# Kernel optimization log

Hardware: AMD Instinct MI355X
Metric: run time of the kernel (lower is better)

Reference implementation:

```python
import jax, jax.numpy as jnp
import numpy as np

B, T, C, H = 2, 2048, 1024, 16
HD = C // H  # head dim = 64


def setup_inputs() -> dict:
    key = jax.random.key(0)
    k1, k2, k3 = jax.random.split(key, 3)
    x = jax.random.normal(k1, (B, T, C), dtype=jnp.float32)
    W_attn = jax.random.normal(k2, (C, 3 * C), dtype=jnp.float32) * (C ** -0.5)
    W_proj = jax.random.normal(k3, (C, C), dtype=jnp.float32) * (C ** -0.5)
    b_proj = jnp.zeros((C,), dtype=jnp.float32)
    return {"x": x, "W_attn": W_attn, "W_proj": W_proj, "b_proj": b_proj}


def reference(x, W_attn, W_proj, b_proj):
    Bv, Tv, Cv = x.shape
    qkv = x @ W_attn  # [B, T, 3C]  (no bias: config.bias=False)
    # NOTE: source splits as k, q, v (k first!)
    k, q, v = jnp.split(qkv, 3, axis=2)
    # [B, H, T, HD]
    q = q.reshape(Bv, Tv, H, HD).transpose(0, 2, 1, 3)
    k = k.reshape(Bv, Tv, H, HD).transpose(0, 2, 1, 3)
    v = v.reshape(Bv, Tv, H, HD).transpose(0, 2, 1, 3)
    wei = jnp.einsum('bhqd,bhkd->bhqk', q, k) * (HD ** -0.5)
    causal = jnp.tril(jnp.ones((Tv, Tv), dtype=bool))
    wei = jnp.where(causal, wei, -jnp.inf)
    wei = jax.nn.softmax(wei, axis=-1)
    # dropout = 0.0 (eval) -> identity
    out = jnp.einsum('bhqk,bhkd->bhqd', wei, v)
    out = out.transpose(0, 2, 1, 3).reshape(Bv, Tv, Cv)
    out = out @ W_proj + b_proj
    return out
```

## Files before the change

### kernel.cpp

```cpp
#include <hip/hip_runtime.h>

typedef __attribute__((ext_vector_type(8))) short short8;
typedef __attribute__((ext_vector_type(4))) short short4v;
typedef __attribute__((ext_vector_type(4))) float float4v;

#define T_SEQ 2048
#define CDIM 1024
#define NHEAD 16
#define HDIM 64
#define PROW 72

__device__ __forceinline__ unsigned short f2bf(float f) {
    unsigned u = __builtin_bit_cast(unsigned, f);
    u += 0x7FFF + ((u >> 16) & 1);
    return (unsigned short)(u >> 16);
}

__device__ __forceinline__ void gload16(const unsigned short* g,
                                        unsigned short* l) {
    __builtin_amdgcn_global_load_lds(
        (const __attribute__((address_space(1))) unsigned int*)g,
        (__attribute__((address_space(3))) unsigned int*)l, 16, 0, 0);
}

__device__ __forceinline__ void phase_barrier() {
    __builtin_amdgcn_sched_barrier(0);
    __builtin_amdgcn_s_barrier();
    __builtin_amdgcn_sched_barrier(0);
}

__global__ __launch_bounds__(256) void preproc(
    const float* __restrict__ x, unsigned short* __restrict__ xb,
    const float* __restrict__ Wa, unsigned short* __restrict__ WaT,
    const float* __restrict__ Wp, unsigned short* __restrict__ WpT) {
    int bid = blockIdx.x, tid = threadIdx.x;
    if (bid < 4096) {
        int i = bid * 256 + tid;
        float4 v = ((const float4*)x)[i];
        ushort4 o;
        o.x = f2bf(v.x); o.y = f2bf(v.y); o.z = f2bf(v.z); o.w = f2bf(v.w);
        ((ushort4*)xb)[i] = o;
        return;
    }
    __shared__ float tile[32][33];
    const float* in;
    unsigned short* out;
    int N, b;
    if (bid < 4096 + 3072) {
        b = bid - 4096; in = Wa; out = WaT; N = 3072;
    } else {
        b = bid - 7168; in = Wp; out = WpT; N = 1024;
    }
    const int K = 1024;
    int kb = (b & 31) * 32, nb = (b >> 5) * 32;
    int tx = tid & 31, ty = tid >> 5;
    for (int r = 0; r < 4; r++)
        tile[ty + r * 8][tx] = in[(size_t)(kb + ty + r * 8) * N + nb + tx];
    __syncthreads();
    for (int r = 0; r < 4; r++)
        out[(size_t)(nb + ty + r * 8) * K + kb + tx] = f2bf(tile[tx][ty + r * 8]);
}

__global__ __launch_bounds__(512) void gemm_qkv(
    const unsigned short* __restrict__ A, const unsigned short* __restrict__ Bt,
    unsigned short* __restrict__ dK, unsigned short* __restrict__ dQ,
    unsigned short* __restrict__ dV) {
    const int K = 1024;
    const int NITER = K / 32;
    __shared__ unsigned short sA[3][128 * 32];
    __shared__ unsigned short sB[3][128 * 32];
    int tid = threadIdx.x, wave = tid >> 6, lane = tid & 63;
    int quad = lane >> 4, l16 = lane & 15;
    int wm = wave >> 1, wn = wave & 1;
    int blockM = blockIdx.y * 128, blockN = blockIdx.x * 128;
    bool swapAB = (blockN >= 2048);

    const unsigned short* gA = A + (size_t)blockM * K;
    const unsigned short* gB = Bt + (size_t)blockN * K;

    int srow = wave * 16 + (lane >> 2);
    int scol = (lane & 3) * 8;
    const unsigned short* pa = gA + (size_t)srow * K + scol;
    const unsigned short* pb = gB + (size_t)srow * K + scol;
    int lo = (wave * 16) * 32;

    float4v acc[2][4] = {};
    int aoff = (wm * 32 + l16) * 32 + quad * 8;
    int boff = (wn * 64 + l16) * 32 + quad * 8;

    for (int t = 0; t < 2; t++) {
        int kb = t * 32;
        gload16(pa + kb, sA[t] + lo);
        gload16(pb + kb, sB[t] + lo);
    }
    asm volatile("s_waitcnt vmcnt(2)" ::: "memory");
    phase_barrier();

#pragma unroll
    for (int it = 0; it < NITER; it++) {
        int cur = it % 3;
        if (it + 2 < NITER) {
            int kb = (it + 2) * 32;
            int nb = (it + 2) % 3;
            gload16(pa + kb, sA[nb] + lo);
            gload16(pb + kb, sB[nb] + lo);
        }
        const unsigned short* cA = sA[cur];
        const unsigned short* cB = sB[cur];
        short8 af[2], bf[4];
        for (int i = 0; i < 2; i++)
            af[i] = *(const short8*)(cA + aoff + i * 16 * 32);
        for (int j = 0; j < 4; j++)
            bf[j] = *(const short8*)(cB + boff + j * 16 * 32);
        if (!swapAB) {
            for (int i = 0; i < 2; i++)
                for (int j = 0; j < 4; j++)
                    acc[i][j] = __builtin_amdgcn_mfma_f32_16x16x32_bf16(
                        af[i], bf[j], acc[i][j], 0, 0, 0);
        } else {
            for (int i = 0; i < 2; i++)
                for (int j = 0; j < 4; j++)
                    acc[i][j] = __builtin_amdgcn_mfma_f32_16x16x32_bf16(
                        bf[j], af[i], acc[i][j], 0, 0, 0);
        }
        if (it + 1 < NITER) {
            if (it + 2 < NITER) {
                asm volatile("s_waitcnt vmcnt(2)" ::: "memory");
            } else {
                asm volatile("s_waitcnt vmcnt(0)" ::: "memory");
            }
            phase_barrier();
        }
    }

    if (!swapAB) {
        const float QSCL = 0.18033688011112042f;
        for (int i = 0; i < 2; i++)
            for (int j = 0; j < 4; j++)
                for (int r = 0; r < 4; r++) {
                    int m = blockM + wm * 32 + i * 16 + quad * 4 + r;
                    int n = blockN + wn * 64 + j * 16 + l16;
                    int part = n >> 10, c = n & 1023;
                    int h = c >> 6, d = c & 63;
                    int bb = m >> 11, t = m & 2047;
                    int bh = bb * NHEAD + h;
                    if (part == 0) {
                        dK[(((size_t)bh * T_SEQ + t) << 6) + d] = f2bf(acc[i][j][r]);
                    } else {
                        dQ[(((size_t)bh * T_SEQ + t) << 6) + d] =
                            f2bf(acc[i][j][r] * QSCL);
                    }
                }
    } else {
        for (int i = 0; i < 2; i++)
            for (int j = 0; j < 4; j++)
                for (int r = 0; r < 4; r++) {
                    int n = blockN + wn * 64 + j * 16 + quad * 4 + r;
                    int m = blockM + wm * 32 + i * 16 + l16;
                    int c = n & 1023;
                    int h = c >> 6, d = c & 63;
                    int bb = m >> 11, t = m & 2047;
                    int bh = bb * NHEAD + h;
                    dV[((size_t)bh * HDIM + d) * T_SEQ + t] = f2bf(acc[i][j][r]);
                }
    }
}

__global__ __launch_bounds__(256) void gemm_proj(
    const unsigned short* __restrict__ A, const unsigned short* __restrict__ Bt,
    const float* __restrict__ bias, float* __restrict__ out) {
    const int K = 1024;
    const int NITER = K / 64;
    __shared__ unsigned short sA[2][64 * PROW];
    __shared__ unsigned short sB[2][64 * PROW];
    int tid = threadIdx.x, wave = tid >> 6, lane = tid & 63;
    int quad = lane >> 4, l16 = lane & 15;
    int wm = wave >> 1, wn = wave & 1;
    int blockM = blockIdx.y * 64, blockN = blockIdx.x * 64;

    int srow = tid >> 3;
    int sseg = tid & 7;
    const unsigned short* gA0 = A + (size_t)(blockM + srow) * K + sseg * 8;
    const unsigned short* gA1 = gA0 + (size_t)32 * K;
    const unsigned short* gB0 = Bt + (size_t)(blockN + srow) * K + sseg * 8;
    const unsigned short* gB1 = gB0 + (size_t)32 * K;
    int so0 = srow * PROW + sseg * 8;
    int so1 = (srow + 32) * PROW + sseg * 8;

    float4v acc[2][2] = {};
    uint4 ra0, ra1, rb0, rb1;

    ra0 = *(const uint4*)gA0; ra1 = *(const uint4*)gA1;
    rb0 = *(const uint4*)gB0; rb1 = *(const uint4*)gB1;
    *(uint4*)(sA[0] + so0) = ra0;
    *(uint4*)(sA[0] + so1) = ra1;
    *(uint4*)(sB[0] + so0) = rb0;
    *(uint4*)(sB[0] + so1) = rb1;

    int aoff = (wm * 32 + l16) * PROW + quad * 8;
    int boff = (wn * 32 + l16) * PROW + quad * 8;

    for (int it = 0; it < NITER; it++) {
        int cur = it & 1;
        __syncthreads();
        if (it + 1 < NITER) {
            int kb = (it + 1) * 64;
            ra0 = *(const uint4*)(gA0 + kb); ra1 = *(const uint4*)(gA1 + kb);
            rb0 = *(const uint4*)(gB0 + kb); rb1 = *(const uint4*)(gB1 + kb);
        }
        const unsigned short* cA = sA[cur];
        const unsigned short* cB = sB[cur];
        short8 af[2][2], bf[2][2];
        for (int i = 0; i < 2; i++)
            for (int k = 0; k < 2; k++)
                af[i][k] = *(const short8*)(cA + aoff + i * 16 * PROW + k * 32);
        for (int j = 0; j < 2; j++)
            for (int k = 0; k < 2; k++)
                bf[j][k] = *(const short8*)(cB + boff + j * 16 * PROW + k * 32);
        for (int i = 0; i < 2; i++)
            for (int j = 0; j < 2; j++) {
                acc[i][j] = __builtin_amdgcn_mfma_f32_16x16x32_bf16(
                    af[i][0], bf[j][0], acc[i][j], 0, 0, 0);
                acc[i][j] = __builtin_amdgcn_mfma_f32_16x16x32_bf16(
                    af[i][1], bf[j][1], acc[i][j], 0, 0, 0);
            }
        if (it + 1 < NITER) {
            int nxt = cur ^ 1;
            *(uint4*)(sA[nxt] + so0) = ra0;
            *(uint4*)(sA[nxt] + so1) = ra1;
            *(uint4*)(sB[nxt] + so0) = rb0;
            *(uint4*)(sB[nxt] + so1) = rb1;
        }
    }

    for (int i = 0; i < 2; i++)
        for (int j = 0; j < 2; j++)
            for (int r = 0; r < 4; r++) {
                int m = blockM + wm * 32 + i * 16 + quad * 4 + r;
                int n = blockN + wn * 32 + j * 16 + l16;
                out[(size_t)m * CDIM + n] = acc[i][j][r] + bias[n];
            }
}

__global__ __launch_bounds__(256) void attn_fwd(
    const unsigned short* __restrict__ Qp, const unsigned short* __restrict__ Kp,
    const unsigned short* __restrict__ Vt, unsigned short* __restrict__ att) {
    __shared__ unsigned short sK[2][64 * 72];
    __shared__ unsigned short sV[2][64 * 72];
    int tid = threadIdx.x, wave = tid >> 6, lane = tid & 63;
    int quad = lane >> 4, l16 = lane & 15;
    int bh = blockIdx.x;
    int bb = bh >> 4, h = bh & 15;
    size_t baseQ = (size_t)bh * T_SEQ * HDIM;
    size_t baseV = (size_t)bh * HDIM * T_SEQ;
    int row4 = tid >> 2, seg = tid & 3;

    int xt = 31 - blockIdx.y;
    int qb = xt * 64;
    int qrow = qb + wave * 16 + l16;

    const unsigned short* qr = Qp + baseQ + (size_t)qrow * HDIM;
    short8 qf0 = *(const short8*)(qr + quad * 8);
    short8 qf1 = *(const short8*)(qr + 32 + quad * 8);

    float4v o[4] = {};
    float lsum = 0.f;
    int nt = xt + 1;

    uint4 ka, kb2, va, vb;
    {
        const unsigned short* gk = Kp + baseQ + (size_t)row4 * HDIM + seg * 16;
        const unsigned short* gv = Vt + baseV + (size_t)row4 * T_SEQ + seg * 16;
        ka = *(const uint4*)gk; kb2 = *(const uint4*)(gk + 8);
        va = *(const uint4*)gv; vb = *(const uint4*)(gv + 8);
    }
    *(uint4*)(sK[0] + row4 * 72 + seg * 16) = ka;
    *(uint4*)(sK[0] + row4 * 72 + seg * 16 + 8) = kb2;
    *(uint4*)(sV[0] + row4 * 72 + seg * 16) = va;
    *(uint4*)(sV[0] + row4 * 72 + seg * 16 + 8) = vb;

    const float4v NEG16 = {-16.f, -16.f, -16.f, -16.f};

    for (int t = 0; t < nt; t++) {
        int cur = t & 1;
        __syncthreads();
        if (t + 1 < nt) {
            const unsigned short* gk =
                Kp + baseQ + (size_t)((t + 1) * 64 + row4) * HDIM + seg * 16;
            const unsigned short* gv =
                Vt + baseV + (size_t)row4 * T_SEQ + (t + 1) * 64 + seg * 16;
            ka = *(const uint4*)gk; kb2 = *(const uint4*)(gk + 8);
            va = *(const uint4*)gv; vb = *(const uint4*)(gv + 8);
        }

        const unsigned short* cK = sK[cur];
        const unsigned short* cV = sV[cur];
        float4v s[4];
        __builtin_amdgcn_s_setprio(1);
        for (int sub = 0; sub < 4; sub++) {
            short8 kf0 = *(const short8*)(cK + (sub * 16 + l16) * 72 + quad * 8);
            short8 kf1 =
                *(const short8*)(cK + (sub * 16 + l16) * 72 + 32 + quad * 8);
            float4v z = NEG16;
            z = __builtin_amdgcn_mfma_f32_16x16x32_bf16(kf0, qf0, z, 0, 0, 0);
            z = __builtin_amdgcn_mfma_f32_16x16x32_bf16(kf1, qf1, z, 0, 0, 0);
            s[sub] = z;
        }
        __builtin_amdgcn_s_setprio(0);

        float e[16];
        bool need_mask = (t * 64 + 63) > (qb + wave * 16);
        if (need_mask) {
            int kgb = t * 64 + quad * 4;
            for (int sub = 0; sub < 4; sub++)
                for (int r = 0; r < 4; r++) {
                    float v = __builtin_amdgcn_exp2f(s[sub][r]);
                    v = (kgb + sub * 16 + r <= qrow) ? v : 0.0f;
                    e[sub * 4 + r] = v;
                    lsum += v;
                }
        } else {
            for (int sub = 0; sub < 4; sub++)
                for (int r = 0; r < 4; r++) {
                    float v = __builtin_amdgcn_exp2f(s[sub][r]);
                    e[sub * 4 + r] = v;
                    lsum += v;
                }
        }

        __builtin_amdgcn_s_setprio(1);
        for (int sub = 0; sub < 4; sub++) {
            unsigned lo, hi;
            asm("v_cvt_pk_bf16_f32 %0, %1, %2"
                : "=v"(lo) : "v"(e[sub * 4 + 0]), "v"(e[sub * 4 + 1]));
            asm("v_cvt_pk_bf16_f32 %0, %1, %2"
                : "=v"(hi) : "v"(e[sub * 4 + 2]), "v"(e[sub * 4 + 3]));
            uint2 packed = {lo, hi};
            short4v pf = __builtin_bit_cast(short4v, packed);
            for (int dc = 0; dc < 4; dc++) {
                short4v vf = *(const short4v*)(
                    cV + (dc * 16 + l16) * 72 + sub * 16 + quad * 4);
                o[dc] = __builtin_amdgcn_mfma_f32_16x16x16bf16_1k(
                    vf, pf, o[dc], 0, 0, 0);
            }
        }
        __builtin_amdgcn_s_setprio(0);

        if (t + 1 < nt) {
            int nxt = cur ^ 1;
            *(uint4*)(sK[nxt] + row4 * 72 + seg * 16) = ka;
            *(uint4*)(sK[nxt] + row4 * 72 + seg * 16 + 8) = kb2;
            *(uint4*)(sV[nxt] + row4 * 72 + seg * 16) = va;
            *(uint4*)(sV[nxt] + row4 * 72 + seg * 16 + 8) = vb;
        }
    }

    lsum += __shfl_xor(lsum, 16);
    lsum += __shfl_xor(lsum, 32);
    float inv = 1.0f / lsum;

    __syncthreads();
    for (int dc = 0; dc < 4; dc++) {
        short4v ov;
        for (int r = 0; r < 4; r++) ov[r] = (short)f2bf(o[dc][r] * inv);
        *(short4v*)(sK[0] + wave * 1152 + l16 * 72 + dc * 16 + quad * 4) = ov;
    }
    __syncthreads();
    int orow = lane >> 2, oseg = lane & 3;
    uint4 a = *(const uint4*)(sK[0] + wave * 1152 + orow * 72 + oseg * 16);
    uint4 b = *(const uint4*)(sK[0] + wave * 1152 + orow * 72 + oseg * 16 + 8);
    unsigned short* dst = att +
        (size_t)(bb * T_SEQ + qb + wave * 16 + orow) * CDIM + h * HDIM +
        oseg * 16;
    *(uint4*)dst = a;
    *(uint4*)(dst + 8) = b;
}

extern "C" void kernel_launch(void* const* d_in, const int* in_sizes, int n_in,
                              void* d_out, int out_size, void* d_ws, size_t ws_size,
                              hipStream_t stream) {
    const float* x      = (const float*)d_in[0];
    const float* W_attn = (const float*)d_in[1];
    const float* W_proj = (const float*)d_in[2];
    const float* b_proj = (const float*)d_in[3];
    float* out = (float*)d_out;

    unsigned short* xb   = (unsigned short*)d_ws;
    unsigned short* WaT  = xb  + 4096 * 1024;
    unsigned short* WpT  = WaT + 3072 * 1024;
    unsigned short* Karr = WpT + 1024 * 1024;
    unsigned short* Qarr = Karr + 2 * 16 * 2048 * 64;
    unsigned short* Varr = Qarr + 2 * 16 * 2048 * 64;
    unsigned short* attb = Varr + 2 * 16 * 2048 * 64;

    preproc<<<8192, 256, 0, stream>>>(x, xb, W_attn, WaT, W_proj, WpT);
    gemm_qkv<<<dim3(24, 32), 512, 0, stream>>>(xb, WaT, Karr, Qarr, Varr);
    attn_fwd<<<dim3(32, 32), 256, 0, stream>>>(Qarr, Karr, Varr, attb);
    gemm_proj<<<dim3(16, 64), 256, 0, stream>>>(attb, WpT, b_proj, out);
}
```

Baseline: 180.4 us.

## Split attention KV loop across two wave groups and merge partial sums

The attention kernel now launches 512 threads per block. Two groups of four waves each process alternating 64-key tiles for the same 64 query rows, and each group keeps its own double-buffered K/V tiles in shared memory. The partial outputs and row sums are combined through shared memory before normalising and writing. This is meant to halve the serial KV loop length per block and add latency hiding, at the cost of doubled LDS use, an extra reduction step, and idle iterations when the tile count is odd.

```diff
diff --git a/kernel.cpp b/kernel.cpp
--- a/kernel.cpp
+++ b/kernel.cpp
@@ -242,22 +242,24 @@
             }
 }
 
-__global__ __launch_bounds__(256) void attn_fwd(
+__global__ __launch_bounds__(512) void attn_fwd(
     const unsigned short* __restrict__ Qp, const unsigned short* __restrict__ Kp,
     const unsigned short* __restrict__ Vt, unsigned short* __restrict__ att) {
-    __shared__ unsigned short sK[2][64 * 72];
-    __shared__ unsigned short sV[2][64 * 72];
+    __shared__ unsigned short sK[2][2][64 * 72];
+    __shared__ unsigned short sV[2][2][64 * 72];
     int tid = threadIdx.x, wave = tid >> 6, lane = tid & 63;
     int quad = lane >> 4, l16 = lane & 15;
+    int half = wave >> 2, qw = wave & 3;
     int bh = blockIdx.x;
     int bb = bh >> 4, h = bh & 15;
     size_t baseQ = (size_t)bh * T_SEQ * HDIM;
     size_t baseV = (size_t)bh * HDIM * T_SEQ;
-    int row4 = tid >> 2, seg = tid & 3;
+    int htid = tid & 255;
+    int row4 = htid >> 2, seg = htid & 3;
 
     int xt = 31 - blockIdx.y;
     int qb = xt * 64;
-    int qrow = qb + wave * 16 + l16;
+    int qrow = qb + qw * 16 + l16;
 
     const unsigned short* qr = Qp + baseQ + (size_t)qrow * HDIM;
     short8 qf0 = *(const short8*)(qr + quad * 8);
@@ -266,114 +268,136 @@
     float4v o[4] = {};
     float lsum = 0.f;
     int nt = xt + 1;
+    int NI = (nt + 1) >> 1;
+
+    const float4v NEG16 = {-16.f, -16.f, -16.f, -16.f};
 
     uint4 ka, kb2, va, vb;
-    {
-        const unsigned short* gk = Kp + baseQ + (size_t)row4 * HDIM + seg * 16;
-        const unsigned short* gv = Vt + baseV + (size_t)row4 * T_SEQ + seg * 16;
+    if (half < nt) {
+        const unsigned short* gk =
+            Kp + baseQ + (size_t)(half * 64 + row4) * HDIM + seg * 16;
+        const unsigned short* gv =
+            Vt + baseV + (size_t)row4 * T_SEQ + half * 64 + seg * 16;
         ka = *(const uint4*)gk; kb2 = *(const uint4*)(gk + 8);
         va = *(const uint4*)gv; vb = *(const uint4*)(gv + 8);
-    }
-    *(uint4*)(sK[0] + row4 * 72 + seg * 16) = ka;
-    *(uint4*)(sK[0] + row4 * 72 + seg * 16 + 8) = kb2;
-    *(uint4*)(sV[0] + row4 * 72 + seg * 16) = va;
-    *(uint4*)(sV[0] + row4 * 72 + seg * 16 + 8) = vb;
-
-    const float4v NEG16 = {-16.f, -16.f, -16.f, -16.f};
-
-    for (int t = 0; t < nt; t++) {
-        int cur = t & 1;
+        *(uint4*)(sK[half][0] + row4 * 72 + seg * 16) = ka;
+        *(uint4*)(sK[half][0] + row4 * 72 + seg * 16 + 8) = kb2;
+        *(uint4*)(sV[half][0] + row4 * 72 + seg * 16) = va;
+        *(uint4*)(sV[half][0] + row4 * 72 + seg * 16 + 8) = vb;
+    }
+
+    for (int i = 0; i < NI; i++) {
+        int t = 2 * i + half;
+        int cur = i & 1;
         __syncthreads();
-        if (t + 1 < nt) {
+        int tn = t + 2;
+        if (tn < nt) {
             const unsigned short* gk =
-                Kp + baseQ + (size_t)((t + 1) * 64 + row4) * HDIM + seg * 16;
+                Kp + baseQ + (size_t)(tn * 64 + row4) * HDIM + seg * 16;
             const unsigned short* gv =
-                Vt + baseV + (size_t)row4 * T_SEQ + (t + 1) * 64 + seg * 16;
+                Vt + baseV + (size_t)row4 * T_SEQ + tn * 64 + seg * 16;
             ka = *(const uint4*)gk; kb2 = *(const uint4*)(gk + 8);
             va = *(const uint4*)gv; vb = *(const uint4*)(gv + 8);
         }
 
-        const unsigned short* cK = sK[cur];
-        const unsigned short* cV = sV[cur];
-        float4v s[4];
-        __builtin_amdgcn_s_setprio(1);
-        for (int sub = 0; sub < 4; sub++) {
-            short8 kf0 = *(const short8*)(cK + (sub * 16 + l16) * 72 + quad * 8);
-            short8 kf1 =
-                *(const short8*)(cK + (sub * 16 + l16) * 72 + 32 + quad * 8);
-            float4v z = NEG16;
-            z = __builtin_amdgcn_mfma_f32_16x16x32_bf16(kf0, qf0, z, 0, 0, 0);
-            z = __builtin_amdgcn_mfma_f32_16x16x32_bf16(kf1, qf1, z, 0, 0, 0);
-            s[sub] = z;
-        }
-        __builtin_amdgcn_s_setprio(0);
-
-        float e[16];
-        bool need_mask = (t * 64 + 63) > (qb + wave * 16);
-        if (need_mask) {
-            int kgb = t * 64 + quad * 4;
-            for (int sub = 0; sub < 4; sub++)
-                for (int r = 0; r < 4; r++) {
-                    float v = __builtin_amdgcn_exp2f(s[sub][r]);
-                    v = (kgb + sub * 16 + r <= qrow) ? v : 0.0f;
-                    e[sub * 4 + r] = v;
-                    lsum += v;
+        if (t < nt) {
+            const unsigned short* cK = sK[half][cur];
+            const unsigned short* cV = sV[half][cur];
+            float4v s[4];
+            __builtin_amdgcn_s_setprio(1);
+            for (int sub = 0; sub < 4; sub++) {
+                short8 kf0 =
+                    *(const short8*)(cK + (sub * 16 + l16) * 72 + quad * 8);
+                short8 kf1 =
+                    *(const short8*)(cK + (sub * 16 + l16) * 72 + 32 + quad * 8);
+                float4v z = NEG16;
+                z = __builtin_amdgcn_mfma_f32_16x16x32_bf16(kf0, qf0, z, 0, 0, 0);
+                z = __builtin_amdgcn_mfma_f32_16x16x32_bf16(kf1, qf1, z, 0, 0, 0);
+                s[sub] = z;
+            }
+            __builtin_amdgcn_s_setprio(0);
+
+            float e[16];
+            bool need_mask = (t * 64 + 63) > (qb + qw * 16);
+            if (need_mask) {
+                int kgb = t * 64 + quad * 4;
+                for (int sub = 0; sub < 4; sub++)
+                    for (int r = 0; r < 4; r++) {
+                        float v = __builtin_amdgcn_exp2f(s[sub][r]);
+                        v = (kgb + sub * 16 + r <= qrow) ? v : 0.0f;
+                        e[sub * 4 + r] = v;
+                        lsum += v;
+                    }
+            } else {
+                for (int sub = 0; sub < 4; sub++)
+                    for (int r = 0; r < 4; r++) {
+                        float v = __builtin_amdgcn_exp2f(s[sub][r]);
+                        e[sub * 4 + r] = v;
+                        lsum += v;
+                    }
+            }
+
+            __builtin_amdgcn_s_setprio(1);
+            for (int sub = 0; sub < 4; sub++) {
+                unsigned lo, hi;
+                asm("v_cvt_pk_bf16_f32 %0, %1, %2"
+                    : "=v"(lo) : "v"(e[sub * 4 + 0]), "v"(e[sub * 4 + 1]));
+                asm("v_cvt_pk_bf16_f32 %0, %1, %2"
+                    : "=v"(hi) : "v"(e[sub * 4 + 2]), "v"(e[sub * 4 + 3]));
+                uint2 packed = {lo, hi};
+                short4v pf = __builtin_bit_cast(short4v, packed);
+                for (int dc = 0; dc < 4; dc++) {
+                    short4v vf = *(const short4v*)(
+                        cV + (dc * 16 + l16) * 72 + sub * 16 + quad * 4);
+                    o[dc] = __builtin_amdgcn_mfma_f32_16x16x16bf16_1k(
+                        vf, pf, o[dc], 0, 0, 0);
                 }
-        } else {
-            for (int sub = 0; sub < 4; sub++)
-                for (int r = 0; r < 4; r++) {
-                    float v = __builtin_amdgcn_exp2f(s[sub][r]);
-                    e[sub * 4 + r] = v;
-                    lsum += v;
-                }
-        }
-
-        __builtin_amdgcn_s_setprio(1);
-        for (int sub = 0; sub < 4; sub++) {
-            unsigned lo, hi;
-            asm("v_cvt_pk_bf16_f32 %0, %1, %2"
-                : "=v"(lo) : "v"(e[sub * 4 + 0]), "v"(e[sub * 4 + 1]));
-            asm("v_cvt_pk_bf16_f32 %0, %1, %2"
-                : "=v"(hi) : "v"(e[sub * 4 + 2]), "v"(e[sub * 4 + 3]));
-            uint2 packed = {lo, hi};
-            short4v pf = __builtin_bit_cast(short4v, packed);
-            for (int dc = 0; dc < 4; dc++) {
-                short4v vf = *(const short4v*)(
-                    cV + (dc * 16 + l16) * 72 + sub * 16 + quad * 4);
-                o[dc] = __builtin_amdgcn_mfma_f32_16x16x16bf16_1k(
-                    vf, pf, o[dc], 0, 0, 0);
-            }
-        }
-        __builtin_amdgcn_s_setprio(0);
-
-        if (t + 1 < nt) {
+            }
+            __builtin_amdgcn_s_setprio(0);
+        }
+
+        if (tn < nt) {
             int nxt = cur ^ 1;
-            *(uint4*)(sK[nxt] + row4 * 72 + seg * 16) = ka;
-            *(uint4*)(sK[nxt] + row4 * 72 + seg * 16 + 8) = kb2;
-            *(uint4*)(sV[nxt] + row4 * 72 + seg * 16) = va;
-            *(uint4*)(sV[nxt] + row4 * 72 + seg * 16 + 8) = vb;
+            *(uint4*)(sK[half][nxt] + row4 * 72 + seg * 16) = ka;
+            *(uint4*)(sK[half][nxt] + row4 * 72 + seg * 16 + 8) = kb2;
+            *(uint4*)(sV[half][nxt] + row4 * 72 + seg * 16) = va;
+            *(uint4*)(sV[half][nxt] + row4 * 72 + seg * 16 + 8) = vb;
         }
     }
 
     lsum += __shfl_xor(lsum, 16);
     lsum += __shfl_xor(lsum, 32);
-    float inv = 1.0f / lsum;
-
+
+    float* mb = (float*)sK;
+    float* slot = mb + (size_t)(qw * 64 + lane) * 20;
     __syncthreads();
-    for (int dc = 0; dc < 4; dc++) {
-        short4v ov;
-        for (int r = 0; r < 4; r++) ov[r] = (short)f2bf(o[dc][r] * inv);
-        *(short4v*)(sK[0] + wave * 1152 + l16 * 72 + dc * 16 + quad * 4) = ov;
+    if (half == 1) {
+        for (int dc = 0; dc < 4; dc++) *(float4v*)(slot + dc * 4) = o[dc];
+        slot[16] = lsum;
     }
     __syncthreads();
-    int orow = lane >> 2, oseg = lane & 3;
-    uint4 a = *(const uint4*)(sK[0] + wave * 1152 + orow * 72 + oseg * 16);
-    uint4 b = *(const uint4*)(sK[0] + wave * 1152 + orow * 72 + oseg * 16 + 8);
-    unsigned short* dst = att +
-        (size_t)(bb * T_SEQ + qb + wave * 16 + orow) * CDIM + h * HDIM +
-        oseg * 16;
-    *(uint4*)dst = a;
-    *(uint4*)(dst + 8) = b;
+    unsigned short* rp = sV[0][0];
+    if (half == 0) {
+        for (int dc = 0; dc < 4; dc++) o[dc] += *(const float4v*)(slot + dc * 4);
+        lsum += slot[16];
+        float inv = 1.0f / lsum;
+        for (int dc = 0; dc < 4; dc++) {
+            short4v ov;
+            for (int r = 0; r < 4; r++) ov[r] = (short)f2bf(o[dc][r] * inv);
+            *(short4v*)(rp + qw * 1152 + l16 * 72 + dc * 16 + quad * 4) = ov;
+        }
+    }
+    __syncthreads();
+    if (half == 0) {
+        int orow = lane >> 2, oseg = lane & 3;
+        uint4 a = *(const uint4*)(rp + qw * 1152 + orow * 72 + oseg * 16);
+        uint4 b = *(const uint4*)(rp + qw * 1152 + orow * 72 + oseg * 16 + 8);
+        unsigned short* dst = att +
+            (size_t)(bb * T_SEQ + qb + qw * 16 + orow) * CDIM + h * HDIM +
+            oseg * 16;
+        *(uint4*)dst = a;
+        *(uint4*)(dst + 8) = b;
+    }
 }
 
 extern "C" void kernel_launch(void* const* d_in, const int* in_sizes, int n_in,
@@ -395,6 +419,6 @@
 
     preproc<<<8192, 256, 0, stream>>>(x, xb, W_attn, WaT, W_proj, WpT);
     gemm_qkv<<<dim3(24, 32), 512, 0, stream>>>(xb, WaT, Karr, Qarr, Varr);
-    attn_fwd<<<dim3(32, 32), 256, 0, stream>>>(Qarr, Karr, Varr, attb);
+    attn_fwd<<<dim3(32, 32), 512, 0, stream>>>(Qarr, Karr, Varr, attb);
     gemm_proj<<<dim3(16, 64), 256, 0, stream>>>(attb, WpT, b_proj, out);
 }
```

Result: faster. 175.4 us (-2.8%).
